# Kernel optimization log

Hardware: AMD Instinct MI355X
Metric: run time of the kernel (lower is better)

## Reference

```python
import jax, jax.numpy as jnp
import numpy as np

P_OUT = 2048   # num_output_points
K_NN = 32      # num_neighbors
LEAK = 0.2     # LeakyReLU slope in WeightNet


def setup_inputs() -> dict:
    key = jax.random.key(0)
    k1, k2, k3, k4 = jax.random.split(key, 4)
    B, N, D, Cin, Cout, Cmid = 8, 8192, 3, 128, 256, 16
    return {
        "coordinates": jax.random.uniform(k1, (B, N, D), jnp.float32),
        "features": jax.random.normal(k2, (B, N, Cin), jnp.float32),
        "wn_w": jax.random.normal(k3, (Cmid, D), jnp.float32) * 0.1,
        "wn_b": jnp.zeros((Cmid,), jnp.float32),
        "lin_w": jax.random.normal(k4, (Cout, Cin * Cmid), jnp.float32) * 0.02,
        "lin_b": jnp.zeros((Cout,), jnp.float32),
    }


def _fps(coords, num_out):
    """Deterministic farthest point sampling (initial point = index 0)."""
    B, N, _ = coords.shape

    def step(carry, _):
        dist, far = carry
        centroid = jnp.take_along_axis(coords, far[:, None, None], axis=1)  # (B,1,D)
        d = jnp.linalg.norm(coords - centroid, axis=-1)                     # (B,N)
        dist = jnp.minimum(dist, d)
        return (dist, jnp.argmax(dist, axis=-1)), far

    init = (jnp.full((B, N), 1e10, coords.dtype), jnp.zeros((B,), jnp.int32))
    _, idx = jax.lax.scan(step, init, None, length=num_out)
    return jnp.transpose(idx)  # (B, num_out)


def _knn(k, coords, centers):
    # squared L2 via gram trick; monotone in L2 so top-k indices match torch.cdist+topk
    d2 = (jnp.sum(centers ** 2, -1)[:, :, None]
          + jnp.sum(coords ** 2, -1)[:, None, :]
          - 2.0 * jnp.einsum('bpd,bnd->bpn', centers, coords))
    _, idx = jax.lax.top_k(-d2, k)
    return idx  # (B,P,K)


_gather = jax.vmap(lambda pts, idx: pts[idx])  # index_points equivalent


def reference(coordinates, features, wn_w, wn_b, lin_w, lin_b):
    B = coordinates.shape[0]
    samp_idx = _fps(coordinates, P_OUT)                      # (B,P)
    out_coords = _gather(coordinates, samp_idx)              # (B,P,D)
    nbr_idx = _knn(K_NN, coordinates, out_coords)            # (B,P,K)
    group_coords = _gather(coordinates, nbr_idx)             # (B,P,K,D)
    centered = group_coords - out_coords[:, :, None, :]      # (B,P,K,D)
    group_feat = _gather(features, nbr_idx)                  # (B,P,K,Cin)
    # WeightNet: 1x1-conv MLP (single layer) + LeakyReLU(0.2)
    w = jax.nn.leaky_relu(jnp.einsum('bpkd,md->bpkm', centered, wn_w) + wn_b, LEAK)
    # PointConv aggregation: (B,P,Cin,K) @ (B,P,K,Cmid) -> (B,P,Cin,Cmid) -> flatten
    nf = jnp.einsum('bpkc,bpkm->bpcm', group_feat, w).reshape(B, P_OUT, -1)
    nf = nf @ lin_w.T + lin_b                                # (B,P,Cout)
    return out_coords, nf
```

## Files before the change

kernel.cpp:

```cpp
#include <hip/hip_runtime.h>
#include <hip/hip_bf16.h>

#define NB    8
#define NPTS  8192
#define P_OUT 2048
#define KNN   32
#define CIN   128
#define CMID  16
#define COUT  256

typedef __bf16 bf16x8 __attribute__((ext_vector_type(8)));
typedef float  f32x4  __attribute__((ext_vector_type(4)));
typedef float  f32x2  __attribute__((ext_vector_type(2)));

__device__ __forceinline__ float sqrt_rn_f32(float x) { return (float)sqrt((double)x); }

__device__ __forceinline__ unsigned short f2bf(float x) {
    unsigned u = __float_as_uint(x);
    return (unsigned short)((u + 0x7FFFu + ((u >> 16) & 1u)) >> 16);
}

__device__ __forceinline__ float wave_max_dpp(float x) {
    int v, t;
    v = __float_as_int(x);
    t = __builtin_amdgcn_update_dpp(v, v, 0xB1, 0xF, 0xF, false);
    x = fmaxf(x, __int_as_float(t));
    v = __float_as_int(x);
    t = __builtin_amdgcn_update_dpp(v, v, 0x4E, 0xF, 0xF, false);
    x = fmaxf(x, __int_as_float(t));
    v = __float_as_int(x);
    t = __builtin_amdgcn_update_dpp(v, v, 0x141, 0xF, 0xF, false);
    x = fmaxf(x, __int_as_float(t));
    v = __float_as_int(x);
    t = __builtin_amdgcn_update_dpp(v, v, 0x140, 0xF, 0xF, false);
    x = fmaxf(x, __int_as_float(t));
    v = __float_as_int(x);
    t = __builtin_amdgcn_update_dpp(v, v, 0x142, 0xA, 0xF, false);
    x = fmaxf(x, __int_as_float(t));
    v = __float_as_int(x);
    t = __builtin_amdgcn_update_dpp(v, v, 0x143, 0xC, 0xF, false);
    x = fmaxf(x, __int_as_float(t));
    return x;
}

__global__ __launch_bounds__(256) void prep_kernel(const float* __restrict__ coords,
                                                   const float* __restrict__ lin_w,
                                                   float2* __restrict__ zp,
                                                   unsigned short* __restrict__ lwbf) {
    const int i = blockIdx.x * 256 + threadIdx.x;
    if (i < NB * NPTS) {
        const float* pc = coords + (size_t)i * 3;
        const float x = pc[0], y = pc[1], z = pc[2];
        float t = __fmul_rn(x, x);
        t = __fadd_rn(t, __fmul_rn(y, y));
        t = __fadd_rn(t, __fmul_rn(z, z));
        zp[i] = make_float2(z, t);
    }
    if (i < COUT * CIN * CMID) lwbf[i] = f2bf(lin_w[i]);
}

__global__ __launch_bounds__(512) void fps_kernel(const float* __restrict__ coords,
                                                  float* __restrict__ out_coords) {
    #pragma clang fp contract(off)
    const int b    = blockIdx.x;
    const int tid  = threadIdx.x;
    const int lane = tid & 63;
    const int wv   = tid >> 6;
    const float* cb = coords + (size_t)b * (NPTS * 3);
    float* outc = out_coords + (size_t)b * (P_OUT * 3);

    __shared__ __align__(16) float warr[8];
    __shared__ unsigned winslot[2];

    f32x2 pxv[8], pyv[8], pzv[8], d2v[8];
    {
        float buf[48];
        const float4* g4 = (const float4*)cb;
        #pragma unroll
        for (int i = 0; i < 12; ++i) {
            float4 v = g4[tid * 12 + i];
            buf[i*4+0] = v.x; buf[i*4+1] = v.y; buf[i*4+2] = v.z; buf[i*4+3] = v.w;
        }
        #pragma unroll
        for (int i = 0; i < 8; ++i) {
            pxv[i] = f32x2{buf[(2*i)*3+0], buf[(2*i+1)*3+0]};
            pyv[i] = f32x2{buf[(2*i)*3+1], buf[(2*i+1)*3+1]};
            pzv[i] = f32x2{buf[(2*i)*3+2], buf[(2*i+1)*3+2]};
            d2v[i] = f32x2{__builtin_inff(), __builtin_inff()};
        }
    }
    if (tid == 0) { winslot[0] = 0xFFFFFFFFu; winslot[1] = 0xFFFFFFFFu; }
    float cx = cb[0], cy = cb[1], cz = cb[2];
    __syncthreads();
    const unsigned base = (unsigned)tid * 16;

    for (int s = 0; s < P_OUT; ++s) {
        if (tid == 0) { outc[s*3+0] = cx; outc[s*3+1] = cy; outc[s*3+2] = cz; }
        if (s == P_OUT - 1) break;

        const f32x2 cx2 = {cx, cx}, cy2 = {cy, cy}, cz2 = {cz, cz};
        f32x2 tmax2 = {0.0f, 0.0f};
        #pragma unroll
        for (int i = 0; i < 8; ++i) {
            const f32x2 dx = pxv[i] - cx2;
            const f32x2 dy = pyv[i] - cy2;
            const f32x2 dz = pzv[i] - cz2;
            f32x2 t = dx * dx;
            t = t + dy * dy;
            t = t + dz * dz;
            const f32x2 nd = __builtin_elementwise_min(d2v[i], t);
            d2v[i] = nd;
            tmax2 = __builtin_elementwise_max(tmax2, nd);
        }
        const float tmax = fmaxf(tmax2[0], tmax2[1]);

        const float wmaxl = wave_max_dpp(tmax);
        if (lane == 63) warr[wv] = wmaxl;
        const float wmax = __shfl(wmaxl, 63, 64);

        const unsigned wb = __float_as_uint(wmax);
        const float s_sp = sqrt_rn_f32(wmax);
        float t_lo_sp = wmax;
        #pragma unroll
        for (int j = 1; j <= 3; ++j) {
            const float v = __uint_as_float(wb - j);
            if (sqrt_rn_f32(v) == s_sp) t_lo_sp = v;
        }
        __syncthreads();
        if (tid == 0) winslot[(s + 1) & 1] = 0xFFFFFFFFu;

        const float4 q0 = *(const float4*)(warr + 0);
        const float4 q1 = *(const float4*)(warr + 4);
        const float gmax = fmaxf(fmaxf(fmaxf(q0.x, q0.y), fmaxf(q0.z, q0.w)),
                                 fmaxf(fmaxf(q1.x, q1.y), fmaxf(q1.z, q1.w)));

        if (wb + 3u >= __float_as_uint(gmax)) {
            float t_lo;
            if (wmax == gmax) {
                t_lo = t_lo_sp;
            } else {
                const float s_ = sqrt_rn_f32(gmax);
                const unsigned gb = __float_as_uint(gmax);
                t_lo = gmax;
                #pragma unroll
                for (int j = 1; j <= 3; ++j) {
                    const float v = __uint_as_float(gb - j);
                    if (sqrt_rn_f32(v) == s_) t_lo = v;
                }
            }
            unsigned cand = 0xFFFFFFFFu;
            #pragma unroll
            for (int i = 7; i >= 0; --i) {
                if (d2v[i][1] >= t_lo) cand = base + 2*i + 1;
                if (d2v[i][0] >= t_lo) cand = base + 2*i;
            }
            if (cand != 0xFFFFFFFFu) atomicMin(&winslot[s & 1], cand);
        }
        __syncthreads();

        const unsigned widx = winslot[s & 1];
        cx = cb[widx * 3 + 0];
        cy = cb[widx * 3 + 1];
        cz = cb[widx * 3 + 2];
    }
}

__global__ __launch_bounds__(1024) void knn_kernel(const float* __restrict__ coords,
                                                   const float2* __restrict__ zp,
                                                   const float* __restrict__ out_coords,
                                                   int* __restrict__ nbr) {
    const int b     = blockIdx.x & 7;
    const int chunk = blockIdx.x >> 3;
    const int tid   = threadIdx.x;
    const int wv    = tid >> 6, lane = tid & 63;
    __shared__ float2 sxy[NPTS];
    {
        float buf[24];
        const float4* g4 = (const float4*)(coords + (size_t)b * (NPTS * 3));
        #pragma unroll
        for (int i = 0; i < 6; ++i) {
            float4 v = g4[tid * 6 + i];
            buf[i*4+0]=v.x; buf[i*4+1]=v.y; buf[i*4+2]=v.z; buf[i*4+3]=v.w;
        }
        #pragma unroll
        for (int i = 0; i < 8; ++i)
            sxy[tid*8 + i] = make_float2(buf[i*3+0], buf[i*3+1]);
    }
    __syncthreads();
    const float2* zpb = zp + (size_t)b * NPTS;

    for (int ci = 0; ci < 4; ++ci) {
        const int p = chunk * 64 + wv * 4 + ci;
        const float* oc = out_coords + ((size_t)b * P_OUT + p) * 3;
        const float cx = oc[0], cy = oc[1], cz = oc[2];
        const float cc = __fadd_rn(__fadd_rn(__fmul_rn(cx,cx), __fmul_rn(cy,cy)), __fmul_rn(cz,cz));
        float ld2 = __builtin_inff();
        unsigned lidx = 0x7FFFFFFFu;
        for (int j0 = 0; j0 < NPTS; j0 += 64) {
            const int p2 = j0 + lane;
            const float2 xy = sxy[p2];
            const float2 zq = zpb[p2];
            const float dot = fmaf(cz, zq.x, fmaf(cy, xy.y, __fmul_rn(cx, xy.x)));
            const float d2  = __fsub_rn(__fadd_rn(cc, zq.y), __fmul_rn(2.0f, dot));
            const float    T  = __shfl(ld2, 31, 64);
            const unsigned Ti = __shfl(lidx, 31, 64);
            const bool qf = (d2 < T) || (d2 == T && (unsigned)p2 < Ti);
            unsigned long long mask = __ballot(qf);
            while (mask) {
                const int l = __ffsll(mask) - 1;
                const float    cd2  = __shfl(d2, l, 64);
                const unsigned cidx = (unsigned)(j0 + l);
                float    pv = __shfl_up(ld2, 1, 64);
                unsigned pi = __shfl_up(lidx, 1, 64);
                if (lane == 0) { pv = cd2; pi = cidx; }
                const bool mlt = (ld2 < cd2) || (ld2 == cd2 && lidx < cidx);
                const bool plt = (pv  < cd2) || (pv  == cd2 && pi   < cidx);
                ld2  = mlt ? ld2  : (plt ? cd2  : pv);
                lidx = mlt ? lidx : (plt ? cidx : pi);
                mask &= (mask - 1);
            }
        }
        if (lane < KNN) nbr[((size_t)b * P_OUT + p) * KNN + lane] = (int)lidx;
    }
}

__global__ __launch_bounds__(128) void pconv_kernel(const float* __restrict__ coords,
                                                    const float* __restrict__ feats,
                                                    const float* __restrict__ out_coords,
                                                    const int* __restrict__ nbr,
                                                    const float* __restrict__ wn_w,
                                                    const float* __restrict__ wn_b,
                                                    unsigned short* __restrict__ nf) {
    const int bp  = (blockIdx.x & 7) * P_OUT + (blockIdx.x >> 3);
    const int b   = bp >> 11;
    const int tid = threadIdx.x;
    __shared__ __align__(16) float wmat[32][16];
    __shared__ int nidx[32];
    __shared__ float ctr[3];
    if (tid < 32) nidx[tid] = nbr[(size_t)bp * KNN + tid];
    if (tid < 3)  ctr[tid]  = out_coords[(size_t)bp * 3 + tid];
    __syncthreads();
    {
        const int k  = tid >> 2;
        const int m0 = (tid & 3) * 4;
        const int n  = nidx[k];
        const float* pc = coords + ((size_t)b * NPTS + n) * 3;
        const float dx = pc[0] - ctr[0];
        const float dy = pc[1] - ctr[1];
        const float dz = pc[2] - ctr[2];
        #pragma unroll
        for (int mm = 0; mm < 4; ++mm) {
            const int m = m0 + mm;
            float a = dx * wn_w[m*3+0] + dy * wn_w[m*3+1] + dz * wn_w[m*3+2] + wn_b[m];
            wmat[k][m] = (a >= 0.0f) ? a : 0.2f * a;
        }
    }
    __syncthreads();
    const int c = tid;
    float acc[16];
    #pragma unroll
    for (int m = 0; m < 16; ++m) acc[m] = 0.0f;
    const float* fb = feats + (size_t)b * NPTS * CIN;
    #pragma unroll 4
    for (int k = 0; k < 32; ++k) {
        const float f = fb[(size_t)nidx[k] * CIN + c];
        const float4* wr = (const float4*)(&wmat[k][0]);
        const float4 w0 = wr[0], w1 = wr[1], w2 = wr[2], w3 = wr[3];
        acc[0]  += f * w0.x;  acc[1]  += f * w0.y;  acc[2]  += f * w0.z;  acc[3]  += f * w0.w;
        acc[4]  += f * w1.x;  acc[5]  += f * w1.y;  acc[6]  += f * w1.z;  acc[7]  += f * w1.w;
        acc[8]  += f * w2.x;  acc[9]  += f * w2.y;  acc[10] += f * w2.z;  acc[11] += f * w2.w;
        acc[12] += f * w3.x;  acc[13] += f * w3.y;  acc[14] += f * w3.z;  acc[15] += f * w3.w;
    }
    unsigned u[8];
    #pragma unroll
    for (int m = 0; m < 8; ++m) {
        const unsigned lo = f2bf(acc[2*m]);
        const unsigned hi = f2bf(acc[2*m+1]);
        u[m] = lo | (hi << 16);
    }
    uint4* dst = (uint4*)(nf + (size_t)bp * 2048 + c * 16);
    dst[0] = make_uint4(u[0], u[1], u[2], u[3]);
    dst[1] = make_uint4(u[4], u[5], u[6], u[7]);
}

__global__ __launch_bounds__(256) void gemm_kernel(const unsigned short* __restrict__ A,
                                                   const unsigned short* __restrict__ Bw,
                                                   const float* __restrict__ bias,
                                                   float* __restrict__ C) {
    __shared__ __align__(16) unsigned short Als[128 * 40];
    __shared__ __align__(16) unsigned short Bls[128 * 40];
    const int tid = threadIdx.x;
    const int m0  = blockIdx.x * 128;
    const int cb  = blockIdx.y;
    const int wv  = tid >> 6, lane = tid & 63;
    const int wr  = wv >> 1,  wc   = wv & 1;
    const int sr  = tid >> 1;
    const int ko  = (tid & 1) * 16;
    const int rr  = lane & 15, kg = lane >> 4;

    f32x4 acc[4][4] = {};

    for (int kt = 0; kt < 2048 / 32; ++kt) {
        const uint4* as = (const uint4*)(A  + (size_t)(m0 + sr) * 2048 + kt * 32 + ko);
        const uint4 a0 = as[0], a1 = as[1];
        const uint4* bs = (const uint4*)(Bw + (size_t)(cb * 128 + sr) * 2048 + kt * 32 + ko);
        const uint4 b0 = bs[0], b1 = bs[1];
        __syncthreads();
        *(uint4*)(&Als[sr * 40 + ko])     = a0;
        *(uint4*)(&Als[sr * 40 + ko + 8]) = a1;
        *(uint4*)(&Bls[sr * 40 + ko])     = b0;
        *(uint4*)(&Bls[sr * 40 + ko + 8]) = b1;
        __syncthreads();
        bf16x8 af[4], bfv[4];
        #pragma unroll
        for (int i = 0; i < 4; ++i)
            af[i] = *(const bf16x8*)(&Als[(wr*64 + i*16 + rr) * 40 + kg * 8]);
        #pragma unroll
        for (int j = 0; j < 4; ++j)
            bfv[j] = *(const bf16x8*)(&Bls[(wc*64 + j*16 + rr) * 40 + kg * 8]);
        #pragma unroll
        for (int i = 0; i < 4; ++i)
            #pragma unroll
            for (int j = 0; j < 4; ++j)
                acc[i][j] = __builtin_amdgcn_mfma_f32_16x16x32_bf16(af[i], bfv[j], acc[i][j], 0, 0, 0);
    }
    const int rg = lane >> 4;
    #pragma unroll
    for (int j = 0; j < 4; ++j) {
        const int col = cb * 128 + wc * 64 + j * 16 + rr;
        const float bv = bias[col];
        #pragma unroll
        for (int i = 0; i < 4; ++i) {
            const int row = m0 + wr * 64 + i * 16 + rg * 4;
            #pragma unroll
            for (int g = 0; g < 4; ++g)
                C[(size_t)(row + g) * 256 + col] = acc[i][j][g] + bv;
        }
    }
}

extern "C" void kernel_launch(void* const* d_in, const int* in_sizes, int n_in,
                              void* d_out, int out_size, void* d_ws, size_t ws_size,
                              hipStream_t stream) {
    const float* coords = (const float*)d_in[0];
    const float* feats  = (const float*)d_in[1];
    const float* wn_w   = (const float*)d_in[2];
    const float* wn_b   = (const float*)d_in[3];
    const float* lin_w  = (const float*)d_in[4];
    const float* lin_b  = (const float*)d_in[5];

    float* out        = (float*)d_out;
    float* out_coords = out;
    float* out_nf     = out + NB * P_OUT * 3;

    char* ws = (char*)d_ws;
    int*            nbr  = (int*)ws;
    float2*         zp   = (float2*)(ws + ((size_t)2  << 20));
    unsigned short* lwbf = (unsigned short*)(ws + ((size_t)2560 << 10));
    unsigned short* nf   = (unsigned short*)(ws + ((size_t)4  << 20));

    prep_kernel <<<2048, 256, 0, stream>>>(coords, lin_w, zp, lwbf);
    fps_kernel  <<<NB, 512, 0, stream>>>(coords, out_coords);
    knn_kernel  <<<256, 1024, 0, stream>>>(coords, zp, out_coords, nbr);
    pconv_kernel<<<NB * P_OUT, 128, 0, stream>>>(coords, feats, out_coords, nbr, wn_w, wn_b, nf);
    gemm_kernel <<<dim3(128, 2), 256, 0, stream>>>(nf, lwbf, lin_b, out_nf);
}
```

Baseline: 3.048 ms.

## Use single-barrier packed-key atomicMax for FPS argmax with triple-buffered slot

Restructures the per-step farthest-point argmax in the FPS kernel. Each wave now computes its local candidate index and does one 64-bit atomicMax on a packed (sqrt-distance, inverted index) key. This replaces the per-wave max array, second reduction and atomicMin, and cuts two block barriers per step to one through a three-slot rotating buffer. It also keeps sampled centroid coordinates in registers spread across threads and writes them out once at the end, instead of a store by thread 0 on every step. The risk is tie-breaking fidelity, which now depends on comparing rounded sqrt values.

```diff
diff --git a/kernel.cpp b/kernel.cpp
--- a/kernel.cpp
+++ b/kernel.cpp
@@ -40,6 +40,23 @@
     v = __float_as_int(x);
     t = __builtin_amdgcn_update_dpp(v, v, 0x143, 0xC, 0xF, false);
     x = fmaxf(x, __int_as_float(t));
+    return x;
+}
+
+__device__ __forceinline__ unsigned wave_min_dpp_u32(unsigned x) {
+    unsigned t;
+    t = (unsigned)__builtin_amdgcn_update_dpp((int)x, (int)x, 0xB1, 0xF, 0xF, false);
+    x = (t < x) ? t : x;
+    t = (unsigned)__builtin_amdgcn_update_dpp((int)x, (int)x, 0x4E, 0xF, 0xF, false);
+    x = (t < x) ? t : x;
+    t = (unsigned)__builtin_amdgcn_update_dpp((int)x, (int)x, 0x141, 0xF, 0xF, false);
+    x = (t < x) ? t : x;
+    t = (unsigned)__builtin_amdgcn_update_dpp((int)x, (int)x, 0x140, 0xF, 0xF, false);
+    x = (t < x) ? t : x;
+    t = (unsigned)__builtin_amdgcn_update_dpp((int)x, (int)x, 0x142, 0xA, 0xF, false);
+    x = (t < x) ? t : x;
+    t = (unsigned)__builtin_amdgcn_update_dpp((int)x, (int)x, 0x143, 0xC, 0xF, false);
+    x = (t < x) ? t : x;
     return x;
 }
 
@@ -65,12 +82,10 @@
     const int b    = blockIdx.x;
     const int tid  = threadIdx.x;
     const int lane = tid & 63;
-    const int wv   = tid >> 6;
     const float* cb = coords + (size_t)b * (NPTS * 3);
     float* outc = out_coords + (size_t)b * (P_OUT * 3);
 
-    __shared__ __align__(16) float warr[8];
-    __shared__ unsigned winslot[2];
+    __shared__ unsigned long long gkey[3];
 
     f32x2 pxv[8], pyv[8], pzv[8], d2v[8];
     {
@@ -89,13 +104,21 @@
             d2v[i] = f32x2{__builtin_inff(), __builtin_inff()};
         }
     }
-    if (tid == 0) { winslot[0] = 0xFFFFFFFFu; winslot[1] = 0xFFFFFFFFu; }
+    if (tid == 0) { gkey[0] = 0ull; gkey[1] = 0ull; gkey[2] = 0ull; }
     float cx = cb[0], cy = cb[1], cz = cb[2];
     __syncthreads();
     const unsigned base = (unsigned)tid * 16;
 
+    float h0x=0,h0y=0,h0z=0, h1x=0,h1y=0,h1z=0, h2x=0,h2y=0,h2z=0, h3x=0,h3y=0,h3z=0;
+
     for (int s = 0; s < P_OUT; ++s) {
-        if (tid == 0) { outc[s*3+0] = cx; outc[s*3+1] = cy; outc[s*3+2] = cz; }
+        if ((s & 511) == tid) {
+            const int k = s >> 9;
+            if      (k == 0) { h0x=cx; h0y=cy; h0z=cz; }
+            else if (k == 1) { h1x=cx; h1y=cy; h1z=cz; }
+            else if (k == 2) { h2x=cx; h2y=cy; h2z=cz; }
+            else             { h3x=cx; h3y=cy; h3z=cz; }
+        }
         if (s == P_OUT - 1) break;
 
         const f32x2 cx2 = {cx, cx}, cy2 = {cy, cy}, cz2 = {cz, cz};
@@ -115,53 +138,47 @@
         const float tmax = fmaxf(tmax2[0], tmax2[1]);
 
         const float wmaxl = wave_max_dpp(tmax);
-        if (lane == 63) warr[wv] = wmaxl;
-        const float wmax = __shfl(wmaxl, 63, 64);
+        const float wmax  = __shfl(wmaxl, 63, 64);
 
         const unsigned wb = __float_as_uint(wmax);
-        const float s_sp = sqrt_rn_f32(wmax);
-        float t_lo_sp = wmax;
+        const float s_ = sqrt_rn_f32(wmax);
+        float t_lo = wmax;
         #pragma unroll
         for (int j = 1; j <= 3; ++j) {
             const float v = __uint_as_float(wb - j);
-            if (sqrt_rn_f32(v) == s_sp) t_lo_sp = v;
+            if (sqrt_rn_f32(v) == s_) t_lo = v;
+        }
+
+        unsigned cand = 0xFFFFFFFFu;
+        #pragma unroll
+        for (int i = 7; i >= 0; --i) {
+            if (d2v[i][1] >= t_lo) cand = base + 2*i + 1;
+            if (d2v[i][0] >= t_lo) cand = base + 2*i;
+        }
+        const unsigned candw = wave_min_dpp_u32(cand);
+        if (lane == 63) {
+            const unsigned long long key =
+                ((unsigned long long)__float_as_uint(s_) << 32) | (unsigned long long)(~candw);
+            atomicMax(&gkey[s % 3], key);
         }
         __syncthreads();
-        if (tid == 0) winslot[(s + 1) & 1] = 0xFFFFFFFFu;
-
-        const float4 q0 = *(const float4*)(warr + 0);
-        const float4 q1 = *(const float4*)(warr + 4);
-        const float gmax = fmaxf(fmaxf(fmaxf(q0.x, q0.y), fmaxf(q0.z, q0.w)),
-                                 fmaxf(fmaxf(q1.x, q1.y), fmaxf(q1.z, q1.w)));
-
-        if (wb + 3u >= __float_as_uint(gmax)) {
-            float t_lo;
-            if (wmax == gmax) {
-                t_lo = t_lo_sp;
-            } else {
-                const float s_ = sqrt_rn_f32(gmax);
-                const unsigned gb = __float_as_uint(gmax);
-                t_lo = gmax;
-                #pragma unroll
-                for (int j = 1; j <= 3; ++j) {
-                    const float v = __uint_as_float(gb - j);
-                    if (sqrt_rn_f32(v) == s_) t_lo = v;
-                }
-            }
-            unsigned cand = 0xFFFFFFFFu;
-            #pragma unroll
-            for (int i = 7; i >= 0; --i) {
-                if (d2v[i][1] >= t_lo) cand = base + 2*i + 1;
-                if (d2v[i][0] >= t_lo) cand = base + 2*i;
-            }
-            if (cand != 0xFFFFFFFFu) atomicMin(&winslot[s & 1], cand);
-        }
-        __syncthreads();
-
-        const unsigned widx = winslot[s & 1];
+
+        if (tid == 0) gkey[(s + 2) % 3] = 0ull;
+
+        const unsigned long long g = gkey[s % 3];
+        const unsigned widx = ~((unsigned)g);
         cx = cb[widx * 3 + 0];
         cy = cb[widx * 3 + 1];
         cz = cb[widx * 3 + 2];
+    }
+
+    #pragma unroll
+    for (int k = 0; k < 4; ++k) {
+        const int s = tid + 512 * k;
+        const float x = (k==0)?h0x:(k==1)?h1x:(k==2)?h2x:h3x;
+        const float y = (k==0)?h0y:(k==1)?h1y:(k==2)?h2y:h3y;
+        const float z = (k==0)?h0z:(k==1)?h1z:(k==2)?h2z:h3z;
+        outc[s*3+0] = x; outc[s*3+1] = y; outc[s*3+2] = z;
     }
 }
 
```

After: 3.392 ms. +11.3%, slower.

## Shrink FPS block to 4 waves, buffer outputs in registers, closed-form sqrt preimage

Applied to the files above, without the earlier changes.

The farthest-point-sampling kernel now runs with 256 threads, so each thread holds 32 points and the cross-wave max reduction covers 4 wave slots instead of 8. Sampled centroids are kept in per-thread registers and written out once after the loop, so the serial loop no longer issues a global store every step. The three-step search for the sqrt tie-threshold is replaced by a closed-form double-precision preimage computation, and the broadcast uses readlane instead of a shuffle. The aim is to cut the per-iteration latency of this serial 2048-step loop (barriers, reduction, stores). The cost is double the per-thread distance work and higher register pressure.

```diff
diff --git a/kernel.cpp b/kernel.cpp
--- a/kernel.cpp
+++ b/kernel.cpp
@@ -14,6 +14,17 @@
 typedef float  f32x2  __attribute__((ext_vector_type(2)));
 
 __device__ __forceinline__ float sqrt_rn_f32(float x) { return (float)sqrt((double)x); }
+
+__device__ __forceinline__ float preimage_min(float s_) {
+    const unsigned sb = __float_as_uint(s_);
+    if (sb == 0u) return 0.0f;
+    const double sd  = (double)s_;
+    const double pd  = (double)__uint_as_float(sb - 1u);
+    const double mid = 0.5 * (sd + pd);
+    const double bb  = mid * mid;
+    const float  fl  = (float)bb;
+    return ((double)fl > bb) ? fl : __uint_as_float(__float_as_uint(fl) + 1u);
+}
 
 __device__ __forceinline__ unsigned short f2bf(float x) {
     unsigned u = __float_as_uint(x);
@@ -59,7 +70,7 @@
     if (i < COUT * CIN * CMID) lwbf[i] = f2bf(lin_w[i]);
 }
 
-__global__ __launch_bounds__(512) void fps_kernel(const float* __restrict__ coords,
+__global__ __launch_bounds__(256) void fps_kernel(const float* __restrict__ coords,
                                                   float* __restrict__ out_coords) {
     #pragma clang fp contract(off)
     const int b    = blockIdx.x;
@@ -69,20 +80,20 @@
     const float* cb = coords + (size_t)b * (NPTS * 3);
     float* outc = out_coords + (size_t)b * (P_OUT * 3);
 
-    __shared__ __align__(16) float warr[8];
+    __shared__ __align__(16) float warr[4];
     __shared__ unsigned winslot[2];
 
-    f32x2 pxv[8], pyv[8], pzv[8], d2v[8];
+    f32x2 pxv[16], pyv[16], pzv[16], d2v[16];
     {
-        float buf[48];
+        float buf[96];
         const float4* g4 = (const float4*)cb;
         #pragma unroll
-        for (int i = 0; i < 12; ++i) {
-            float4 v = g4[tid * 12 + i];
+        for (int i = 0; i < 24; ++i) {
+            float4 v = g4[tid * 24 + i];
             buf[i*4+0] = v.x; buf[i*4+1] = v.y; buf[i*4+2] = v.z; buf[i*4+3] = v.w;
         }
         #pragma unroll
-        for (int i = 0; i < 8; ++i) {
+        for (int i = 0; i < 16; ++i) {
             pxv[i] = f32x2{buf[(2*i)*3+0], buf[(2*i+1)*3+0]};
             pyv[i] = f32x2{buf[(2*i)*3+1], buf[(2*i+1)*3+1]};
             pzv[i] = f32x2{buf[(2*i)*3+2], buf[(2*i+1)*3+2]};
@@ -92,16 +103,29 @@
     if (tid == 0) { winslot[0] = 0xFFFFFFFFu; winslot[1] = 0xFFFFFFFFu; }
     float cx = cb[0], cy = cb[1], cz = cb[2];
     __syncthreads();
-    const unsigned base = (unsigned)tid * 16;
+    const unsigned base = (unsigned)tid * 32;
+
+    float h0x=0,h0y=0,h0z=0, h1x=0,h1y=0,h1z=0, h2x=0,h2y=0,h2z=0, h3x=0,h3y=0,h3z=0;
+    float h4x=0,h4y=0,h4z=0, h5x=0,h5y=0,h5z=0, h6x=0,h6y=0,h6z=0, h7x=0,h7y=0,h7z=0;
 
     for (int s = 0; s < P_OUT; ++s) {
-        if (tid == 0) { outc[s*3+0] = cx; outc[s*3+1] = cy; outc[s*3+2] = cz; }
+        if ((s & 255) == tid) {
+            const int k = s >> 8;
+            if      (k == 0) { h0x=cx; h0y=cy; h0z=cz; }
+            else if (k == 1) { h1x=cx; h1y=cy; h1z=cz; }
+            else if (k == 2) { h2x=cx; h2y=cy; h2z=cz; }
+            else if (k == 3) { h3x=cx; h3y=cy; h3z=cz; }
+            else if (k == 4) { h4x=cx; h4y=cy; h4z=cz; }
+            else if (k == 5) { h5x=cx; h5y=cy; h5z=cz; }
+            else if (k == 6) { h6x=cx; h6y=cy; h6z=cz; }
+            else             { h7x=cx; h7y=cy; h7z=cz; }
+        }
         if (s == P_OUT - 1) break;
 
         const f32x2 cx2 = {cx, cx}, cy2 = {cy, cy}, cz2 = {cz, cz};
         f32x2 tmax2 = {0.0f, 0.0f};
         #pragma unroll
-        for (int i = 0; i < 8; ++i) {
+        for (int i = 0; i < 16; ++i) {
             const f32x2 dx = pxv[i] - cx2;
             const f32x2 dy = pyv[i] - cy2;
             const f32x2 dz = pzv[i] - cz2;
@@ -116,41 +140,23 @@
 
         const float wmaxl = wave_max_dpp(tmax);
         if (lane == 63) warr[wv] = wmaxl;
-        const float wmax = __shfl(wmaxl, 63, 64);
+        const float wmax = __int_as_float(__builtin_amdgcn_readlane(__float_as_int(wmaxl), 63));
 
         const unsigned wb = __float_as_uint(wmax);
-        const float s_sp = sqrt_rn_f32(wmax);
-        float t_lo_sp = wmax;
-        #pragma unroll
-        for (int j = 1; j <= 3; ++j) {
-            const float v = __uint_as_float(wb - j);
-            if (sqrt_rn_f32(v) == s_sp) t_lo_sp = v;
-        }
+        const float t_lo_sp = preimage_min(sqrt_rn_f32(wmax));
         __syncthreads();
         if (tid == 0) winslot[(s + 1) & 1] = 0xFFFFFFFFu;
 
-        const float4 q0 = *(const float4*)(warr + 0);
-        const float4 q1 = *(const float4*)(warr + 4);
-        const float gmax = fmaxf(fmaxf(fmaxf(q0.x, q0.y), fmaxf(q0.z, q0.w)),
-                                 fmaxf(fmaxf(q1.x, q1.y), fmaxf(q1.z, q1.w)));
+        const float4 q0 = *(const float4*)(warr);
+        const float gmax = fmaxf(fmaxf(q0.x, q0.y), fmaxf(q0.z, q0.w));
 
         if (wb + 3u >= __float_as_uint(gmax)) {
-            float t_lo;
-            if (wmax == gmax) {
-                t_lo = t_lo_sp;
-            } else {
-                const float s_ = sqrt_rn_f32(gmax);
-                const unsigned gb = __float_as_uint(gmax);
-                t_lo = gmax;
-                #pragma unroll
-                for (int j = 1; j <= 3; ++j) {
-                    const float v = __uint_as_float(gb - j);
-                    if (sqrt_rn_f32(v) == s_) t_lo = v;
-                }
-            }
+            const float t_lo = (wmax == gmax)
+                             ? t_lo_sp
+                             : preimage_min(sqrt_rn_f32(gmax));
             unsigned cand = 0xFFFFFFFFu;
             #pragma unroll
-            for (int i = 7; i >= 0; --i) {
+            for (int i = 15; i >= 0; --i) {
                 if (d2v[i][1] >= t_lo) cand = base + 2*i + 1;
                 if (d2v[i][0] >= t_lo) cand = base + 2*i;
             }
@@ -162,6 +168,21 @@
         cx = cb[widx * 3 + 0];
         cy = cb[widx * 3 + 1];
         cz = cb[widx * 3 + 2];
+    }
+
+    #pragma unroll
+    for (int kk = 0; kk < 8; ++kk) {
+        const int s = tid + 256 * kk;
+        float x, y, z;
+        if      (kk == 0) { x=h0x; y=h0y; z=h0z; }
+        else if (kk == 1) { x=h1x; y=h1y; z=h1z; }
+        else if (kk == 2) { x=h2x; y=h2y; z=h2z; }
+        else if (kk == 3) { x=h3x; y=h3y; z=h3z; }
+        else if (kk == 4) { x=h4x; y=h4y; z=h4z; }
+        else if (kk == 5) { x=h5x; y=h5y; z=h5z; }
+        else if (kk == 6) { x=h6x; y=h6y; z=h6z; }
+        else              { x=h7x; y=h7y; z=h7z; }
+        outc[s*3+0] = x; outc[s*3+1] = y; outc[s*3+2] = z;
     }
 }
 
@@ -360,7 +381,7 @@
     unsigned short* nf   = (unsigned short*)(ws + ((size_t)4  << 20));
 
     prep_kernel <<<2048, 256, 0, stream>>>(coords, lin_w, zp, lwbf);
-    fps_kernel  <<<NB, 512, 0, stream>>>(coords, out_coords);
+    fps_kernel  <<<NB, 256, 0, stream>>>(coords, out_coords);
     knn_kernel  <<<256, 1024, 0, stream>>>(coords, zp, out_coords, nbr);
     pconv_kernel<<<NB * P_OUT, 128, 0, stream>>>(coords, feats, out_coords, nbr, wn_w, wn_b, nf);
     gemm_kernel <<<dim3(128, 2), 256, 0, stream>>>(nf, lwbf, lin_b, out_nf);
```

Measured after the change: 2.866 ms. -6.0%, faster.
